# Kernel tuning notes

Measured on AMD Instinct MI355X. Metric: run time of the kernel, lower is better.

Reference implementation:

```python
import jax, jax.numpy as jnp
import numpy as np

RATIO = 2          # BigVGAN Activation1d up/down ratio
K_FILT = 12        # int(6 * ratio // 2) * 2
DILATIONS = (1, 3, 5)


def _kaiser_sinc_filter1d(cutoff, half_width, kernel_size):
    # Faithful port of BigVGAN's kaiser_sinc_filter1d (even kernel path).
    half_size = kernel_size // 2
    delta_f = 4.0 * half_width
    A = 2.285 * (half_size - 1) * np.pi * delta_f + 7.95
    if A > 50.0:
        beta = 0.1102 * (A - 8.7)
    elif A >= 21.0:
        beta = 0.5842 * (A - 21.0) ** 0.4 + 0.07886 * (A - 21.0)
    else:
        beta = 0.0
    window = np.kaiser(kernel_size, beta)              # periodic=False
    time = np.arange(-half_size, half_size) + 0.5       # even kernel size
    filt = 2.0 * cutoff * window * np.sinc(2.0 * cutoff * time)
    filt = filt / filt.sum()
    return jnp.asarray(filt, dtype=jnp.float32)

FILT = _kaiser_sinc_filter1d(0.5 / RATIO, 0.6 / RATIO, K_FILT)


def _depthwise1d(x, filt, stride, lhs_dilation, padding):
    # x: (B, T, C), filt: (k,) shared across channels (depthwise)
    C = x.shape[-1]
    kern = jnp.tile(filt[:, None, None], (1, 1, C))  # (k, 1, C)
    return jax.lax.conv_general_dilated(
        x, kern, window_strides=(stride,), padding=padding,
        lhs_dilation=(lhs_dilation,), feature_group_count=C,
        dimension_numbers=('NLC', 'LIO', 'NLC'))


def upsample2(x):
    # BigVGAN UpSample1d(ratio=2): replicate pad -> conv_transpose -> crop
    pad = K_FILT // RATIO - 1                       # 5
    pad_left = pad * RATIO + (K_FILT - RATIO) // 2  # 15
    pad_right = pad * RATIO + (K_FILT - RATIO + 1) // 2  # 15
    x = jnp.pad(x, ((0, 0), (pad, pad), (0, 0)), mode='edge')
    # conv_transpose(stride=r) == lhs-dilated conv with full padding
    # (filter is symmetric, so no flip needed)
    y = RATIO * _depthwise1d(x, FILT, 1, RATIO, [(K_FILT - 1, K_FILT - 1)])
    return y[:, pad_left:-pad_right, :]  # (B, 2T, C)


def downsample2(x):
    # BigVGAN DownSample1d(ratio=2) == LowPassFilter1d(stride=2)
    pad_left = K_FILT // 2 - 1  # 5 (even kernel)
    pad_right = K_FILT // 2     # 6
    x = jnp.pad(x, ((0, 0), (pad_left, pad_right), (0, 0)), mode='edge')
    return _depthwise1d(x, FILT, RATIO, 1, 'VALID')  # (B, T, C)


def snake(x, log_alpha):
    # alpha_logscale=True: alpha = exp(param); x + (1/alpha) sin^2(alpha x)
    alpha = jnp.exp(log_alpha)  # (C,), broadcasts over (B, T, C)
    return x + (1.0 / (alpha + 1e-9)) * jnp.square(jnp.sin(alpha * x))


def act1d(x, log_alpha):
    return downsample2(snake(upsample2(x), log_alpha))


def wn_conv(x, v, g, b, dilation):
    # weight-norm: kernel = v / ||v||_(0,1) * g, then SAME dilated conv
    norm = jnp.linalg.norm(v, axis=(0, 1))[None, None, :]  # (1,1,Cout)
    kern = (v / norm) * g  # (k, Cin, Cout)
    y = jax.lax.conv_general_dilated(
        x, kern, window_strides=(1,), padding='SAME',
        rhs_dilation=(dilation,), dimension_numbers=('NLC', 'LIO', 'NLC'))
    return y + b


def setup_inputs() -> dict:
    key = jax.random.key(0)
    ks = jax.random.split(key, 7)
    B, T, C, K = 4, 8192, 512, 3
    n = len(DILATIONS)
    x = jax.random.normal(ks[0], (B, T, C), dtype=jnp.float32)
    v1 = jax.random.normal(ks[1], (n, K, C, C), dtype=jnp.float32)
    g1 = jax.random.uniform(ks[2], (n, 1, 1, C), dtype=jnp.float32)
    b1 = 0.01 * jax.random.normal(ks[3], (n, C), dtype=jnp.float32)
    v2 = jax.random.normal(ks[4], (n, K, C, C), dtype=jnp.float32)
    g2 = jax.random.uniform(ks[5], (n, 1, 1, C), dtype=jnp.float32)
    b2 = 0.01 * jax.random.normal(ks[6], (n, C), dtype=jnp.float32)
    alphas = jnp.zeros((2 * n, C), dtype=jnp.float32)  # log-alpha init 0
    return {'x': x, 'v1': v1, 'g1': g1, 'b1': b1,
            'v2': v2, 'g2': g2, 'b2': b2, 'alphas': alphas}


def reference(x, v1, g1, b1, v2, g2, b2, alphas):
    for i, d in enumerate(DILATIONS):
        xt = act1d(x, alphas[2 * i])
        xt = wn_conv(xt, v1[i], g1[i], b1[i], d)
        xt = act1d(xt, alphas[2 * i + 1])
        xt = wn_conv(xt, v2[i], g2[i], b2[i], 1)
        x = xt + x
    return x
```

## Files before the change

kernel.cpp:

```cpp
#include <hip/hip_runtime.h>
#include <math.h>

#define TLEN   8192
#define CCH    512
#define NBATCH 4
#define GUARD_B 8
#define GUARD_T 16
#define XROWS  (TLEN + GUARD_B + GUARD_T)

typedef __attribute__((ext_vector_type(8))) short short8;
typedef __attribute__((ext_vector_type(4))) float f32x4;

struct Filt { float f[12]; };

#define MFMA16(a, b, c) __builtin_amdgcn_mfma_f32_16x16x32_bf16(a, b, c, 0, 0, 0)

__device__ __forceinline__ unsigned short f2bf(float f) {
  unsigned u = __float_as_uint(f);
  unsigned r = (u + 0x7fffu + ((u >> 16) & 1u)) >> 16;
  return (unsigned short)r;
}

__device__ __forceinline__ float fast_sin(float x) {
  float r = x * 0.15915494309189535f;
  r -= floorf(r);
  return __builtin_amdgcn_sinf(r);
}

__device__ __forceinline__ float snake1(float u, float a, float rcp) {
  float s = fast_sin(a * u);
  return fmaf(rcp * s, s, u);
}

__device__ __forceinline__ void gload16(const void* g, void* l) {
  __builtin_amdgcn_global_load_lds(
      (const __attribute__((address_space(1))) unsigned int*)g,
      (__attribute__((address_space(3))) unsigned int*)l, 16, 0, 0);
}

__global__ __launch_bounds__(64)
void scale_k(const float* __restrict__ v1, const float* __restrict__ v2,
             const float* __restrict__ g1, const float* __restrict__ g2,
             float* __restrict__ scl) {
  const int conv = blockIdx.x;
  const int co   = blockIdx.y * 64 + threadIdx.x;
  const float* v = (conv < 3) ? v1 + (size_t)conv * 3 * CCH * CCH
                              : v2 + (size_t)(conv - 3) * 3 * CCH * CCH;
  const float* g = (conv < 3) ? g1 + conv * CCH : g2 + (conv - 3) * CCH;
  float s = 0.f;
  #pragma unroll 8
  for (int j = 0; j < 3 * CCH; ++j) {
    float w = v[(size_t)j * CCH + co];
    s = fmaf(w, w, s);
  }
  scl[conv * CCH + co] = g[co] / sqrtf(s);
}

__global__ __launch_bounds__(512)
void zguard_k(unsigned short* __restrict__ xb) {
  const int b = blockIdx.x / 24;
  const int g = blockIdx.x % 24;
  const int row = (g < 8) ? g : (TLEN + g);
  xb[((size_t)b * XROWS + row) * CCH + threadIdx.x] = 0;
}

__global__ __launch_bounds__(256)
void wprep_k(const float* __restrict__ v1, const float* __restrict__ v2,
             const float* __restrict__ scl, unsigned short* __restrict__ wp) {
  const int gtid = blockIdx.x * 256 + threadIdx.x;
  const int lane = gtid & 63;
  const int gw = gtid >> 6;
  const int c  = gw / 1536;
  int r = gw - c * 1536;
  const int tap = r >> 9;  r &= 511;
  const int cib = r >> 6;  r &= 63;
  const int cob = r >> 4;
  const int cb  = r & 15;
  const int nf = cb >> 1, kk = cb & 1;
  const int co  = cob * 128 + nf * 16 + (lane & 15);
  const int ci0 = cib * 64 + kk * 32 + (lane >> 4) * 8;
  const float* v = (c < 3) ? v1 + (size_t)c * 3 * CCH * CCH
                           : v2 + (size_t)(c - 3) * 3 * CCH * CCH;
  const float s = scl[c * CCH + co];
  unsigned short o[8];
  #pragma unroll
  for (int j = 0; j < 8; ++j) {
    float w = v[((size_t)tap * CCH + ci0 + j) * CCH + co] * s;
    o[j] = f2bf(w);
  }
  *reinterpret_cast<short8*>(wp + (size_t)gw * 512 + lane * 8) =
      *reinterpret_cast<const short8*>(o);
}

__global__ __launch_bounds__(256)
void act_k(const float* __restrict__ x, unsigned short* __restrict__ y,
           const float* __restrict__ la, Filt F) {
  const int idx = blockIdx.x * 256 + threadIdx.x;
  const int c  = (idx & 127) << 2;
  const int ts = (idx >> 7) & 2047;
  const int b  = idx >> 18;
  const int t0 = ts * 4;
  const float* xbp = x + ((size_t)b * TLEN) * CCH + c;

  float av[4], rv[4];
  #pragma unroll
  for (int ch = 0; ch < 4; ++ch) {
    av[ch] = expf(la[c + ch]);
    rv[ch] = 1.f / (av[ch] + 1e-9f);
  }

  float acc[4][4];

  if (ts >= 2 && ts <= 2045) {
    f32x4 xw[14];
    const float* xp = xbp + (size_t)(t0 - 5) * CCH;
    #pragma unroll
    for (int j = 0; j < 14; ++j)
      xw[j] = *reinterpret_cast<const f32x4*>(xp + (size_t)j * CCH);

    #pragma unroll
    for (int ch = 0; ch < 4; ++ch) {
      float s[18];
      #pragma unroll
      for (int mi = 0; mi < 18; ++mi) {
        float u = 0.f;
        if (mi & 1) {
          const int base = (mi - 5) / 2 + 2;
          #pragma unroll
          for (int r = 0; r < 6; ++r) u = fmaf(F.f[2*r], xw[base + r][ch], u);
        } else {
          const int base = (mi - 6) / 2 + 3;
          #pragma unroll
          for (int r = 0; r < 6; ++r) u = fmaf(F.f[2*r+1], xw[base + r][ch], u);
        }
        u *= 2.f;
        s[mi] = snake1(u, av[ch], rv[ch]);
      }
      #pragma unroll
      for (int tt = 0; tt < 4; ++tt) {
        float a = 0.f;
        #pragma unroll
        for (int k = 0; k < 12; ++k) a = fmaf(F.f[k], s[2*tt + k], a);
        acc[tt][ch] = a;
      }
    }
  } else {
    #pragma unroll
    for (int tt = 0; tt < 4; ++tt) {
      const int t = t0 + tt;
      float a0=0.f, a1=0.f, a2=0.f, a3=0.f;
      for (int k = 0; k < 12; ++k) {
        int m  = 2*t + k - 5;
        int mc = m < 0 ? 0 : (m > 2*TLEN - 1 ? 2*TLEN - 1 : m);
        int tp = mc >> 1;
        int odd = mc & 1;
        float u0=0.f,u1=0.f,u2=0.f,u3=0.f;
        #pragma unroll
        for (int r = 0; r < 6; ++r) {
          int i  = odd ? (tp + r - 2) : (tp + r - 3);
          int ic = i < 0 ? 0 : (i > TLEN - 1 ? TLEN - 1 : i);
          float tap = odd ? F.f[2*r+1] : F.f[2*r];
          const float* p = xbp + (size_t)ic * CCH;
          u0 = fmaf(tap, p[0], u0); u1 = fmaf(tap, p[1], u1);
          u2 = fmaf(tap, p[2], u2); u3 = fmaf(tap, p[3], u3);
        }
        u0 *= 2.f; u1 *= 2.f; u2 *= 2.f; u3 *= 2.f;
        const float fk = F.f[k];
        a0 = fmaf(fk, snake1(u0,av[0],rv[0]), a0);
        a1 = fmaf(fk, snake1(u1,av[1],rv[1]), a1);
        a2 = fmaf(fk, snake1(u2,av[2],rv[2]), a2);
        a3 = fmaf(fk, snake1(u3,av[3],rv[3]), a3);
      }
      acc[tt][0]=a0; acc[tt][1]=a1; acc[tt][2]=a2; acc[tt][3]=a3;
    }
  }

  #pragma unroll
  for (int tt = 0; tt < 4; ++tt) {
    ushort4 o;
    o.x = f2bf(acc[tt][0]); o.y = f2bf(acc[tt][1]);
    o.z = f2bf(acc[tt][2]); o.w = f2bf(acc[tt][3]);
    *reinterpret_cast<ushort4*>(
        y + ((size_t)b * XROWS + GUARD_B + t0 + tt) * CCH + c) = o;
  }
}

template<int DIL>
__global__ __launch_bounds__(256)
void convm_k(const unsigned short* __restrict__ xb,
             const unsigned short* __restrict__ wp,
             const float* __restrict__ bia,
             const float* __restrict__ res,
             float* __restrict__ out) {
  __shared__ unsigned short As[2][144 * 64];
  __shared__ unsigned short Bs[2][16 * 512];

  const int tid  = threadIdx.x;
  const int lane = tid & 63;
  const int wid  = tid >> 6;
  const int wr = wid >> 1, wc = wid & 1;

  const int l   = (blockIdx.x & 7) * 128 + (blockIdx.x >> 3);
  const int coB = l & 3;
  const int tb  = l >> 2;
  const int b   = tb >> 6;
  const int t0  = (tb & 63) * 128;
  const int co0 = coB * 128;

  const int qq = lane >> 4;
  const int r0 = lane & 15;

  const int a_r = lane >> 3;
  const int a_c = (lane & 7) ^ a_r;
  const unsigned short* xrow0 =
      xb + ((size_t)b * XROWS + GUARD_B + t0 - DIL) * CCH;

  f32x4 acc[4][4] = {};

  auto stageA = [&](int cib, int buf) {
    #pragma unroll
    for (int u = 0; u < 5; ++u) {
      const int i = wid + u * 4;
      if (i < 18) {
        const unsigned short* g =
            xrow0 + (size_t)(8 * i + a_r) * CCH + cib * 64 + a_c * 8;
        gload16(g, &As[buf][i * 512]);
      }
    }
  };
  auto stageB = [&](int tap, int cib, int buf) {
    #pragma unroll
    for (int u = 0; u < 4; ++u) {
      const int cb = wid * 4 + u;
      const unsigned short* g =
          wp + ((((size_t)(tap * 8 + cib) * 4 + coB) * 16 + cb) * 512) + lane * 8;
      gload16(g, &Bs[buf][cb * 512]);
    }
  };
  auto compute = [&](int tap, int pa, int pb) {
    const int rowbase = tap * DIL + wr * 64 + r0;
    const int xr = (tap * DIL + r0) & 7;
    #pragma unroll
    for (int kk = 0; kk < 2; ++kk) {
      const int coff = 8 * ((kk * 4 + qq) ^ xr);
      short8 af[4], bf[4];
      #pragma unroll
      for (int i = 0; i < 4; ++i)
        af[i] = *reinterpret_cast<const short8*>(
            &As[pa][(rowbase + i * 16) * 64 + coff]);
      #pragma unroll
      for (int j = 0; j < 4; ++j)
        bf[j] = *reinterpret_cast<const short8*>(
            &Bs[pb][((wc * 4 + j) * 2 + kk) * 512 + lane * 8]);
      #pragma unroll
      for (int i = 0; i < 4; ++i)
        #pragma unroll
        for (int j = 0; j < 4; ++j)
          acc[i][j] = MFMA16(af[i], bf[j], acc[i][j]);
    }
  };

  stageA(0, 0);
  stageB(0, 0, 0);
  __syncthreads();

  int pa = 0, pb = 0;
  for (int cib = 0; cib < 8; ++cib) {
    #pragma unroll
    for (int tap = 0; tap < 3; ++tap) {
      if (tap < 2) {
        stageB(tap + 1, cib, pb ^ 1);
      } else if (cib < 7) {
        stageB(0, cib + 1, pb ^ 1);
        stageA(cib + 1, pa ^ 1);
      }
      compute(tap, pa, pb);
      __syncthreads();
      pb ^= 1;
    }
    pa ^= 1;
  }

  #pragma unroll
  for (int j = 0; j < 4; ++j) {
    const int co = co0 + (wc * 4 + j) * 16 + r0;
    const float bv = bia[co];
    #pragma unroll
    for (int i = 0; i < 4; ++i) {
      const int t = t0 + (wr * 4 + i) * 16 + qq * 4;
      #pragma unroll
      for (int e = 0; e < 4; ++e) {
        const size_t off = ((size_t)b * TLEN + t + e) * CCH + co;
        float o = acc[i][j][e] + bv;
        if (res) o += res[off];
        out[off] = o;
      }
    }
  }
}

static double bessel_i0(double x) {
  double t = 1.0, s = 1.0, q = x * x * 0.25;
  for (int k = 1; k < 64; ++k) {
    t *= q / ((double)k * (double)k);
    s += t;
    if (t < 1e-18 * s) break;
  }
  return s;
}

static void make_filter(Filt* F) {
  const double cutoff = 0.25, hw = 0.3;
  const int ks = 12, half = 6;
  const double A = 2.285 * (half - 1) * M_PI * (4.0 * hw) + 7.95;
  double beta;
  if (A > 50.0)       beta = 0.1102 * (A - 8.7);
  else if (A >= 21.0) beta = 0.5842 * pow(A - 21.0, 0.4) + 0.07886 * (A - 21.0);
  else                beta = 0.0;
  const double i0b = bessel_i0(beta);
  double f[12], sum = 0.0;
  for (int n = 0; n < 12; ++n) {
    double rr = 2.0 * n / (ks - 1) - 1.0;
    double w  = bessel_i0(beta * sqrt(fmax(0.0, 1.0 - rr * rr))) / i0b;
    double tm = (double)(n - half) + 0.5;
    double sx = 2.0 * cutoff * tm;
    double snc = (sx == 0.0) ? 1.0 : sin(M_PI * sx) / (M_PI * sx);
    f[n] = 2.0 * cutoff * w * snc;
    sum += f[n];
  }
  for (int n = 0; n < 12; ++n) F->f[n] = (float)(f[n] / sum);
}

extern "C" void kernel_launch(void* const* d_in, const int* in_sizes, int n_in,
                              void* d_out, int out_size, void* d_ws, size_t ws_size,
                              hipStream_t stream) {
  (void)in_sizes; (void)n_in; (void)out_size; (void)ws_size;
  const float* x  = (const float*)d_in[0];
  const float* v1 = (const float*)d_in[1];
  const float* g1 = (const float*)d_in[2];
  const float* b1 = (const float*)d_in[3];
  const float* v2 = (const float*)d_in[4];
  const float* g2 = (const float*)d_in[5];
  const float* b2 = (const float*)d_in[6];
  const float* al = (const float*)d_in[7];
  float* out = (float*)d_out;

  const size_t N = (size_t)NBATCH * TLEN * CCH;
  float* w1 = (float*)d_ws;
  unsigned short* xbuf = (unsigned short*)(w1 + N);
  unsigned short* wp   = xbuf + (size_t)NBATCH * XROWS * CCH;
  float* scl = (float*)(wp + (size_t)6 * 3 * CCH * CCH);

  Filt F;
  make_filter(&F);

  zguard_k<<<96, 512, 0, stream>>>(xbuf);
  scale_k<<<dim3(6, 8), 64, 0, stream>>>(v1, v2, g1, g2, scl);
  wprep_k<<<2304, 256, 0, stream>>>(v1, v2, scl, wp);

  const int cgrid = NBATCH * (TLEN / 128) * 4;
  const int nblk_act = (NBATCH * 2048 * 128) / 256;
  const size_t wsz = (size_t)3 * CCH * CCH;

  for (int i = 0; i < 3; ++i) {
    const float* xsrc = (i == 0) ? x : out;
    act_k<<<nblk_act, 256, 0, stream>>>(xsrc, xbuf, al + (size_t)(2 * i) * CCH, F);
    if (i == 0)
      convm_k<1><<<cgrid, 256, 0, stream>>>(xbuf, wp + 0 * wsz, b1 + 0 * CCH, nullptr, w1);
    else if (i == 1)
      convm_k<3><<<cgrid, 256, 0, stream>>>(xbuf, wp + 1 * wsz, b1 + 1 * CCH, nullptr, w1);
    else
      convm_k<5><<<cgrid, 256, 0, stream>>>(xbuf, wp + 2 * wsz, b1 + 2 * CCH, nullptr, w1);
    act_k<<<nblk_act, 256, 0, stream>>>(w1, xbuf, al + (size_t)(2 * i + 1) * CCH, F);
    convm_k<1><<<cgrid, 256, 0, stream>>>(xbuf, wp + (3 + i) * wsz, b2 + i * CCH, xsrc, out);
  }
}
```

Measured before the change: 798.7 us.

## Restructure conv pipeline, stream A via registers, bf16 intermediates, parallel weight norm

The conv kernel stops staging activations through LDS. Each wave now loads its A fragments straight into registers, and a three-slot B buffer with manual waitcnt and barriers pipelines the loads across taps, with raised MFMA priority and 2 blocks per CU. The intermediate conv output is stored as bf16 instead of fp32, which halves that traffic, and the following activation kernel reads bf16. The weight-norm scale is split into a parallel partial-sum kernel plus a finalize kernel. Risks are extra rounding error from the bf16 intermediate and fragile hand-tuned vmcnt counts.

```diff
diff --git a/kernel.cpp b/kernel.cpp
--- a/kernel.cpp
+++ b/kernel.cpp
@@ -21,6 +21,10 @@
   return (unsigned short)r;
 }
 
+__device__ __forceinline__ float bf2f(unsigned short u) {
+  return __uint_as_float((unsigned)u << 16);
+}
+
 __device__ __forceinline__ float fast_sin(float x) {
   float r = x * 0.15915494309189535f;
   r -= floorf(r);
@@ -38,22 +42,44 @@
       (__attribute__((address_space(3))) unsigned int*)l, 16, 0, 0);
 }
 
-__global__ __launch_bounds__(64)
-void scale_k(const float* __restrict__ v1, const float* __restrict__ v2,
-             const float* __restrict__ g1, const float* __restrict__ g2,
-             float* __restrict__ scl) {
-  const int conv = blockIdx.x;
-  const int co   = blockIdx.y * 64 + threadIdx.x;
-  const float* v = (conv < 3) ? v1 + (size_t)conv * 3 * CCH * CCH
-                              : v2 + (size_t)(conv - 3) * 3 * CCH * CCH;
-  const float* g = (conv < 3) ? g1 + conv * CCH : g2 + (conv - 3) * CCH;
+__global__ __launch_bounds__(256)
+void normp_k(const float* __restrict__ v1, const float* __restrict__ v2,
+             float* __restrict__ part) {
+  __shared__ float red[256];
+  const int c  = blockIdx.x;
+  const int cc = blockIdx.y;
+  const int jc = blockIdx.z;
+  const int col = threadIdx.x & 63;
+  const int js  = threadIdx.x >> 6;
+  const int co = cc * 64 + col;
+  const float* v = (c < 3) ? v1 + (size_t)c * 3 * CCH * CCH
+                           : v2 + (size_t)(c - 3) * 3 * CCH * CCH;
+  const int j0 = jc * 64 + js * 16;
   float s = 0.f;
-  #pragma unroll 8
-  for (int j = 0; j < 3 * CCH; ++j) {
-    float w = v[(size_t)j * CCH + co];
+  #pragma unroll
+  for (int jj = 0; jj < 16; ++jj) {
+    float w = v[(size_t)(j0 + jj) * CCH + co];
     s = fmaf(w, w, s);
   }
-  scl[conv * CCH + co] = g[co] / sqrtf(s);
+  red[threadIdx.x] = s;
+  __syncthreads();
+  if (threadIdx.x < 64) {
+    float t = red[threadIdx.x] + red[threadIdx.x + 64] +
+              red[threadIdx.x + 128] + red[threadIdx.x + 192];
+    part[(size_t)(c * CCH + co) * 24 + jc] = t;
+  }
+}
+
+__global__ __launch_bounds__(256)
+void fin_k(const float* __restrict__ part, const float* __restrict__ g1,
+           const float* __restrict__ g2, float* __restrict__ scl) {
+  const int i = blockIdx.x * 256 + threadIdx.x;
+  const int c = i >> 9, co = i & 511;
+  float s = 0.f;
+  #pragma unroll
+  for (int jc = 0; jc < 24; ++jc) s += part[(size_t)i * 24 + jc];
+  const float g = (c < 3) ? g1[c * CCH + co] : g2[(c - 3) * CCH + co];
+  scl[i] = g / sqrtf(s);
 }
 
 __global__ __launch_bounds__(512)
@@ -92,15 +118,29 @@
       *reinterpret_cast<const short8*>(o);
 }
 
+template<int INBF>
 __global__ __launch_bounds__(256)
-void act_k(const float* __restrict__ x, unsigned short* __restrict__ y,
+void act_k(const void* __restrict__ xin, unsigned short* __restrict__ y,
            const float* __restrict__ la, Filt F) {
   const int idx = blockIdx.x * 256 + threadIdx.x;
   const int c  = (idx & 127) << 2;
   const int ts = (idx >> 7) & 2047;
   const int b  = idx >> 18;
   const int t0 = ts * 4;
-  const float* xbp = x + ((size_t)b * TLEN) * CCH + c;
+
+  auto ldrow = [&](int row) -> f32x4 {
+    if constexpr (INBF) {
+      const unsigned short* p =
+          (const unsigned short*)xin + ((size_t)b * TLEN + row) * CCH + c;
+      ushort4 u = *reinterpret_cast<const ushort4*>(p);
+      f32x4 r;
+      r[0] = bf2f(u.x); r[1] = bf2f(u.y); r[2] = bf2f(u.z); r[3] = bf2f(u.w);
+      return r;
+    } else {
+      const float* p = (const float*)xin + ((size_t)b * TLEN + row) * CCH + c;
+      return *reinterpret_cast<const f32x4*>(p);
+    }
+  };
 
   float av[4], rv[4];
   #pragma unroll
@@ -113,10 +153,8 @@
 
   if (ts >= 2 && ts <= 2045) {
     f32x4 xw[14];
-    const float* xp = xbp + (size_t)(t0 - 5) * CCH;
-    #pragma unroll
-    for (int j = 0; j < 14; ++j)
-      xw[j] = *reinterpret_cast<const f32x4*>(xp + (size_t)j * CCH);
+    #pragma unroll
+    for (int j = 0; j < 14; ++j) xw[j] = ldrow(t0 - 5 + j);
 
     #pragma unroll
     for (int ch = 0; ch < 4; ++ch) {
@@ -160,9 +198,9 @@
           int i  = odd ? (tp + r - 2) : (tp + r - 3);
           int ic = i < 0 ? 0 : (i > TLEN - 1 ? TLEN - 1 : i);
           float tap = odd ? F.f[2*r+1] : F.f[2*r];
-          const float* p = xbp + (size_t)ic * CCH;
-          u0 = fmaf(tap, p[0], u0); u1 = fmaf(tap, p[1], u1);
-          u2 = fmaf(tap, p[2], u2); u3 = fmaf(tap, p[3], u3);
+          f32x4 xv = ldrow(ic);
+          u0 = fmaf(tap, xv[0], u0); u1 = fmaf(tap, xv[1], u1);
+          u2 = fmaf(tap, xv[2], u2); u3 = fmaf(tap, xv[3], u3);
         }
         u0 *= 2.f; u1 *= 2.f; u2 *= 2.f; u3 *= 2.f;
         const float fk = F.f[k];
@@ -185,15 +223,15 @@
   }
 }
 
-template<int DIL>
-__global__ __launch_bounds__(256)
+template<int DIL, int OB>
+__global__ __launch_bounds__(256, 2)
 void convm_k(const unsigned short* __restrict__ xb,
              const unsigned short* __restrict__ wp,
              const float* __restrict__ bia,
              const float* __restrict__ res,
-             float* __restrict__ out) {
-  __shared__ unsigned short As[2][144 * 64];
-  __shared__ unsigned short Bs[2][16 * 512];
+             float* __restrict__ outf,
+             unsigned short* __restrict__ outb) {
+  __shared__ unsigned short Bs[3][16 * 512];
 
   const int tid  = threadIdx.x;
   const int lane = tid & 63;
@@ -210,76 +248,82 @@
   const int qq = lane >> 4;
   const int r0 = lane & 15;
 
-  const int a_r = lane >> 3;
-  const int a_c = (lane & 7) ^ a_r;
-  const unsigned short* xrow0 =
-      xb + ((size_t)b * XROWS + GUARD_B + t0 - DIL) * CCH;
+  const unsigned short* pA =
+      xb + ((size_t)b * XROWS + GUARD_B + t0 - DIL + wr * 64 + r0) * CCH + qq * 8;
 
   f32x4 acc[4][4] = {};
-
-  auto stageA = [&](int cib, int buf) {
-    #pragma unroll
-    for (int u = 0; u < 5; ++u) {
-      const int i = wid + u * 4;
-      if (i < 18) {
-        const unsigned short* g =
-            xrow0 + (size_t)(8 * i + a_r) * CCH + cib * 64 + a_c * 8;
-        gload16(g, &As[buf][i * 512]);
-      }
-    }
+  short8 afr0[8], afr1[8], afr2[8];
+
+  auto loadA = [&](int cib, int tapv, short8* dst) {
+    #pragma unroll
+    for (int i = 0; i < 4; ++i)
+      #pragma unroll
+      for (int kk = 0; kk < 2; ++kk)
+        dst[i * 2 + kk] = *reinterpret_cast<const short8*>(
+            pA + (size_t)(tapv * DIL + i * 16) * CCH + cib * 64 + kk * 32);
   };
-  auto stageB = [&](int tap, int cib, int buf) {
+  auto stageB = [&](int tap, int cib, unsigned short* buf) {
     #pragma unroll
     for (int u = 0; u < 4; ++u) {
       const int cb = wid * 4 + u;
       const unsigned short* g =
           wp + ((((size_t)(tap * 8 + cib) * 4 + coB) * 16 + cb) * 512) + lane * 8;
-      gload16(g, &Bs[buf][cb * 512]);
+      gload16(g, buf + cb * 512);
     }
   };
-  auto compute = [&](int tap, int pa, int pb) {
-    const int rowbase = tap * DIL + wr * 64 + r0;
-    const int xr = (tap * DIL + r0) & 7;
+  auto compute = [&](const short8* af, const unsigned short* bsb) {
+    __builtin_amdgcn_s_setprio(1);
     #pragma unroll
     for (int kk = 0; kk < 2; ++kk) {
-      const int coff = 8 * ((kk * 4 + qq) ^ xr);
-      short8 af[4], bf[4];
-      #pragma unroll
-      for (int i = 0; i < 4; ++i)
-        af[i] = *reinterpret_cast<const short8*>(
-            &As[pa][(rowbase + i * 16) * 64 + coff]);
+      short8 bf[4];
       #pragma unroll
       for (int j = 0; j < 4; ++j)
         bf[j] = *reinterpret_cast<const short8*>(
-            &Bs[pb][((wc * 4 + j) * 2 + kk) * 512 + lane * 8]);
+            &bsb[((wc * 4 + j) * 2 + kk) * 512 + lane * 8]);
       #pragma unroll
       for (int i = 0; i < 4; ++i)
         #pragma unroll
         for (int j = 0; j < 4; ++j)
-          acc[i][j] = MFMA16(af[i], bf[j], acc[i][j]);
-    }
+          acc[i][j] = MFMA16(af[i * 2 + kk], bf[j], acc[i][j]);
+    }
+    __builtin_amdgcn_s_setprio(0);
   };
 
-  stageA(0, 0);
-  stageB(0, 0, 0);
-  __syncthreads();
-
-  int pa = 0, pb = 0;
-  for (int cib = 0; cib < 8; ++cib) {
-    #pragma unroll
-    for (int tap = 0; tap < 3; ++tap) {
-      if (tap < 2) {
-        stageB(tap + 1, cib, pb ^ 1);
-      } else if (cib < 7) {
-        stageB(0, cib + 1, pb ^ 1);
-        stageA(cib + 1, pa ^ 1);
-      }
-      compute(tap, pa, pb);
-      __syncthreads();
-      pb ^= 1;
-    }
-    pa ^= 1;
-  }
+  loadA(0, 0, afr0); stageB(0, 0, Bs[0]);
+  loadA(0, 1, afr1); stageB(1, 0, Bs[1]);
+
+  for (int cib = 0; cib < 7; ++cib) {
+    __builtin_amdgcn_s_barrier();
+    loadA(cib, 2, afr2); stageB(2, cib, Bs[2]);
+    asm volatile("s_waitcnt vmcnt(24)" ::: "memory");
+    __builtin_amdgcn_s_barrier();
+    compute(afr0, Bs[0]);
+    __builtin_amdgcn_s_barrier();
+    loadA(cib + 1, 0, afr0); stageB(0, cib + 1, Bs[0]);
+    asm volatile("s_waitcnt vmcnt(24)" ::: "memory");
+    __builtin_amdgcn_s_barrier();
+    compute(afr1, Bs[1]);
+    __builtin_amdgcn_s_barrier();
+    loadA(cib + 1, 1, afr1); stageB(1, cib + 1, Bs[1]);
+    asm volatile("s_waitcnt vmcnt(24)" ::: "memory");
+    __builtin_amdgcn_s_barrier();
+    compute(afr2, Bs[2]);
+  }
+  __builtin_amdgcn_s_barrier();
+  loadA(7, 2, afr2); stageB(2, 7, Bs[2]);
+  asm volatile("s_waitcnt vmcnt(24)" ::: "memory");
+  __builtin_amdgcn_s_barrier();
+  compute(afr0, Bs[0]);
+
+  __builtin_amdgcn_s_barrier();
+  asm volatile("s_waitcnt vmcnt(12)" ::: "memory");
+  __builtin_amdgcn_s_barrier();
+  compute(afr1, Bs[1]);
+
+  __builtin_amdgcn_s_barrier();
+  asm volatile("s_waitcnt vmcnt(0)" ::: "memory");
+  __builtin_amdgcn_s_barrier();
+  compute(afr2, Bs[2]);
 
   #pragma unroll
   for (int j = 0; j < 4; ++j) {
@@ -292,8 +336,12 @@
       for (int e = 0; e < 4; ++e) {
         const size_t off = ((size_t)b * TLEN + t + e) * CCH + co;
         float o = acc[i][j][e] + bv;
-        if (res) o += res[off];
-        out[off] = o;
+        if constexpr (OB) {
+          outb[off] = f2bf(o);
+        } else {
+          if (res) o += res[off];
+          outf[off] = o;
+        }
       }
     }
   }
@@ -346,16 +394,18 @@
   float* out = (float*)d_out;
 
   const size_t N = (size_t)NBATCH * TLEN * CCH;
-  float* w1 = (float*)d_ws;
-  unsigned short* xbuf = (unsigned short*)(w1 + N);
+  unsigned short* wb1  = (unsigned short*)d_ws;
+  unsigned short* xbuf = wb1 + N;
   unsigned short* wp   = xbuf + (size_t)NBATCH * XROWS * CCH;
-  float* scl = (float*)(wp + (size_t)6 * 3 * CCH * CCH);
+  float* part = (float*)(wp + (size_t)6 * 3 * CCH * CCH);
+  float* scl  = part + (size_t)6 * CCH * 24;
 
   Filt F;
   make_filter(&F);
 
   zguard_k<<<96, 512, 0, stream>>>(xbuf);
-  scale_k<<<dim3(6, 8), 64, 0, stream>>>(v1, v2, g1, g2, scl);
+  normp_k<<<dim3(6, 8, 24), 256, 0, stream>>>(v1, v2, part);
+  fin_k<<<12, 256, 0, stream>>>(part, g1, g2, scl);
   wprep_k<<<2304, 256, 0, stream>>>(v1, v2, scl, wp);
 
   const int cgrid = NBATCH * (TLEN / 128) * 4;
@@ -364,14 +414,18 @@
 
   for (int i = 0; i < 3; ++i) {
     const float* xsrc = (i == 0) ? x : out;
-    act_k<<<nblk_act, 256, 0, stream>>>(xsrc, xbuf, al + (size_t)(2 * i) * CCH, F);
+    act_k<0><<<nblk_act, 256, 0, stream>>>(xsrc, xbuf, al + (size_t)(2 * i) * CCH, F);
     if (i == 0)
-      convm_k<1><<<cgrid, 256, 0, stream>>>(xbuf, wp + 0 * wsz, b1 + 0 * CCH, nullptr, w1);
+      convm_k<1, 1><<<cgrid, 256, 0, stream>>>(xbuf, wp + 0 * wsz, b1 + 0 * CCH,
+                                               nullptr, nullptr, wb1);
     else if (i == 1)
-      convm_k<3><<<cgrid, 256, 0, stream>>>(xbuf, wp + 1 * wsz, b1 + 1 * CCH, nullptr, w1);
+      convm_k<3, 1><<<cgrid, 256, 0, stream>>>(xbuf, wp + 1 * wsz, b1 + 1 * CCH,
+                                               nullptr, nullptr, wb1);
     else
-      convm_k<5><<<cgrid, 256, 0, stream>>>(xbuf, wp + 2 * wsz, b1 + 2 * CCH, nullptr, w1);
-    act_k<<<nblk_act, 256, 0, stream>>>(w1, xbuf, al + (size_t)(2 * i + 1) * CCH, F);
-    convm_k<1><<<cgrid, 256, 0, stream>>>(xbuf, wp + (3 + i) * wsz, b2 + i * CCH, xsrc, out);
-  }
-}
+      convm_k<5, 1><<<cgrid, 256, 0, stream>>>(xbuf, wp + 2 * wsz, b1 + 2 * CCH,
+                                               nullptr, nullptr, wb1);
+    act_k<1><<<nblk_act, 256, 0, stream>>>(wb1, xbuf, al + (size_t)(2 * i + 1) * CCH, F);
+    convm_k<1, 0><<<cgrid, 256, 0, stream>>>(xbuf, wp + (3 + i) * wsz, b2 + i * CCH,
+                                             xsrc, out, nullptr);
+  }
+}
```

Result: slower. 1.010 ms (+26.5%).
